# Optimization experiments

Hardware: AMD Instinct MI355X
Metric: run time of the kernel (lower is better)

## Reference

```python
import jax, jax.numpy as jnp
import numpy as np

N_HEADS = 16


def setup_inputs() -> dict:
    key = jax.random.key(0)
    ks = jax.random.split(key, 4)
    B, S, D = 2, 2048, 1024
    x = jax.random.normal(ks[0], (B, S, D), dtype=jnp.float32)
    scale = 1.0 / np.sqrt(D)
    Wq = jax.random.normal(ks[1], (D, D), dtype=jnp.float32) * scale
    Wk = jax.random.normal(ks[2], (D, D), dtype=jnp.float32) * scale
    Wv = jax.random.normal(ks[3], (D, D), dtype=jnp.float32) * scale
    bq = jnp.zeros((D,), jnp.float32)
    bk = jnp.zeros((D,), jnp.float32)
    bv = jnp.zeros((D,), jnp.float32)
    return {"x": x, "Wq": Wq, "bq": bq, "Wk": Wk, "bk": bk, "Wv": Wv, "bv": bv}


def _split_heads(t, n_heads):
    B, S, D = t.shape
    return t.reshape(B, S, n_heads, D // n_heads).transpose(0, 2, 1, 3)  # [B,H,S,hd]


def reference(x, Wq, bq, Wk, bk, Wv, bv):
    H = N_HEADS
    Q = _split_heads(x @ Wq + bq, H)
    K = _split_heads(x @ Wk + bk, H)
    V = _split_heads(x @ Wv + bv, H)
    head_size = Q.shape[-1]
    scores = jnp.einsum("bhqd,bhkd->bhqk", Q, K) / jnp.sqrt(jnp.float32(head_size))
    probs = jax.nn.softmax(scores, axis=-1)  # dropout p=0.01 -> identity in eval
    out = jnp.einsum("bhqk,bhkd->bhqd", probs, V)
    B, _, S, hd = out.shape
    return out.transpose(0, 2, 1, 3).reshape(B, S, H * hd)
```

## Files before the change

kernel.cpp:

```cpp
#include <hip/hip_runtime.h>
#include <hip/hip_bf16.h>

typedef __bf16 bf16x8 __attribute__((ext_vector_type(8)));
typedef __bf16 bf16x4 __attribute__((ext_vector_type(4)));
typedef float f32x4 __attribute__((ext_vector_type(4)));

#define B_ 2
#define S_ 2048
#define D_ 1024
#define H_ 16
#define HD_ 64
#define NT_ (S_ / 64)

__device__ inline void load_lds16(const __bf16* g, __bf16* l) {
  __builtin_amdgcn_global_load_lds(
      (const __attribute__((address_space(1))) void*)g,
      (__attribute__((address_space(3))) void*)l, 16, 0, 0);
}

__global__ __launch_bounds__(256) void prep(
    const float* __restrict__ X,
    const float* __restrict__ Wq, const float* __restrict__ Wk,
    const float* __restrict__ Wv,
    __bf16* __restrict__ Xb, __bf16* __restrict__ WT)
{
  const int z = blockIdx.z, t = threadIdx.x;
  if (z == 3) {
    size_t base = ((size_t)(blockIdx.y * 16 + blockIdx.x)) * 16384 + t * 4;
#pragma unroll
    for (int i = 0; i < 16; ++i) {
      size_t idx = base + (size_t)i * 1024;
      f32x4 v = *(const f32x4*)(X + idx);
      __bf16 o[4];
#pragma unroll
      for (int j = 0; j < 4; ++j) o[j] = (__bf16)v[j];
      *(ulong1*)(Xb + idx) = *(ulong1*)o;
    }
    return;
  }
  const float* W = (z == 0) ? Wq : (z == 1) ? Wk : Wv;
  __bf16* WTz = WT + (size_t)z * D_ * D_;
  const int k0 = blockIdx.y * 64, n0 = blockIdx.x * 64;

  __shared__ __bf16 T[64 * 72];
  {
    int kl = t >> 2, cg = (t & 3) * 16;
    const float* wp = W + (size_t)(k0 + kl) * D_ + n0 + cg;
    bf16x8 a, b;
#pragma unroll
    for (int j = 0; j < 4; ++j) { a[j] = (__bf16)wp[j];     a[4 + j] = (__bf16)wp[4 + j]; }
#pragma unroll
    for (int j = 0; j < 4; ++j) { b[j] = (__bf16)wp[8 + j]; b[4 + j] = (__bf16)wp[12 + j]; }
    *(bf16x8*)(T + kl * 72 + cg) = a;
    *(bf16x8*)(T + kl * 72 + cg + 8) = b;
  }
  __syncthreads();
  {
    int nl = t >> 2, kc = (t & 3) * 16;
    bf16x8 a, b;
#pragma unroll
    for (int j = 0; j < 8; ++j) a[j] = T[(kc + j) * 72 + nl];
#pragma unroll
    for (int j = 0; j < 8; ++j) b[j] = T[(kc + 8 + j) * 72 + nl];
    __bf16* op = WTz + (size_t)(n0 + nl) * D_ + k0 + kc;
    *(bf16x8*)(op) = a;
    *(bf16x8*)(op + 8) = b;
  }
}

__global__ __launch_bounds__(256) void qkv_gemm(
    const __bf16* __restrict__ Xb, const __bf16* __restrict__ WT,
    const float* __restrict__ bq, const float* __restrict__ bk,
    const float* __restrict__ bv,
    __bf16* __restrict__ Qw, __bf16* __restrict__ Kw, __bf16* __restrict__ VTw)
{
  const int z = blockIdx.z;
  const __bf16* Wz = WT + (size_t)z * D_ * D_;
  const float* bias = (z == 0) ? bq : (z == 1) ? bk : bv;
  __bf16* outp = (z == 0) ? Qw : (z == 1) ? Kw : VTw;
  const float mult = (z == 0) ? 0.125f * 1.44269504088896f : 1.0f;

  const int tid  = threadIdx.x;
  const int wave = tid >> 6, lane = tid & 63, ln = lane & 15, quad = lane >> 4;
  const int m0 = blockIdx.y * 128, n0 = blockIdx.x * 128;
  const int wm = (wave & 1) * 64, wn = (wave >> 1) * 64;

  __shared__ __bf16 Als[128 * 32];
  __shared__ __bf16 Bls[128 * 32];

  f32x4 acc[4][4] = {};

  for (int k0 = 0; k0 < D_; k0 += 32) {
    __syncthreads();
#pragma unroll
    for (int i = 0; i < 2; ++i) {
      int cb = wave * 128 + i * 64;
      int chunk = cb + lane;
      int row = chunk >> 2, c = chunk & 3;
      load_lds16(Xb + (size_t)(m0 + row) * D_ + k0 + c * 8, Als + cb * 8);
      load_lds16(Wz + (size_t)(n0 + row) * D_ + k0 + c * 8, Bls + cb * 8);
    }
    __syncthreads();

    bf16x8 af[4], bfr[4];
#pragma unroll
    for (int mt = 0; mt < 4; ++mt)
      af[mt] = *(const bf16x8*)(Als + (wm + mt * 16 + ln) * 32 + quad * 8);
#pragma unroll
    for (int nt = 0; nt < 4; ++nt)
      bfr[nt] = *(const bf16x8*)(Bls + (wn + nt * 16 + ln) * 32 + quad * 8);
#pragma unroll
    for (int mt = 0; mt < 4; ++mt)
#pragma unroll
      for (int nt = 0; nt < 4; ++nt)
        acc[mt][nt] = __builtin_amdgcn_mfma_f32_16x16x32_bf16(af[mt], bfr[nt], acc[mt][nt], 0, 0, 0);
  }

#pragma unroll
  for (int nt = 0; nt < 4; ++nt) {
    int n_g = n0 + wn + nt * 16 + ln;
    float bv_ = bias[n_g];
#pragma unroll
    for (int mt = 0; mt < 4; ++mt) {
#pragma unroll
      for (int r = 0; r < 4; ++r) {
        int m_g = m0 + wm + mt * 16 + quad * 4 + r;
        float c = (acc[mt][nt][r] + bv_) * mult;
        if (z < 2) {
          outp[(size_t)m_g * D_ + n_g] = (__bf16)c;
        } else {
          outp[(size_t)(m_g >> 11) * D_ * S_ + (size_t)n_g * S_ + (m_g & (S_ - 1))] = (__bf16)c;
        }
      }
    }
  }
}

__global__ __launch_bounds__(256) void attn(
    const __bf16* __restrict__ Q, const __bf16* __restrict__ K,
    const __bf16* __restrict__ VT, float* __restrict__ out)
{
  const int tid  = threadIdx.x;
  const int wave = tid >> 6, lane = tid & 63, ln = lane & 15, quad = lane >> 4;

  const int f = blockIdx.x;
  const int xcd = f & 7, g = f >> 3;
  const int bh = ((g & 3) << 3) | xcd;
  const int qt = g >> 2;
  const int b = bh >> 4, h = bh & 15;
  const int q0 = qt * 128 + wave * 32;

  const __bf16* Qbase = Q + (size_t)(b * S_ + q0) * D_ + h * HD_;
  bf16x8 qb[2][2];
#pragma unroll
  for (int nt = 0; nt < 2; ++nt)
#pragma unroll
    for (int ks = 0; ks < 2; ++ks)
      qb[nt][ks] = *(const bf16x8*)(Qbase + (size_t)(nt * 16 + ln) * D_ + ks * 32 + quad * 8);

  const __bf16* Kh = K + (size_t)b * S_ * D_ + h * HD_;
  const __bf16* Vh = VT + (size_t)(b * D_ + h * HD_) * S_;

  __shared__ __bf16 Kls[2][64 * 72];
  __shared__ __bf16 Vls[2][64 * 72];
  __shared__ __bf16 Pls[4][32 * 72];
  __shared__ float  Linv[4][32];
  __bf16* Pw = Pls[wave];

  f32x4 acc[2][4] = {};
  float lsum[2] = {0.f, 0.f};

  bf16x8 kreg[2], vreg[2];
#pragma unroll
  for (int i = 0; i < 2; ++i) {
    int chunk = i * 256 + tid, row = chunk >> 3, cc = chunk & 7;
    kreg[i] = *(const bf16x8*)(Kh + (size_t)row * D_ + cc * 8);
    vreg[i] = *(const bf16x8*)(Vh + (size_t)row * S_ + cc * 8);
  }

  for (int kt = 0; kt < NT_; ++kt) {
    __bf16* Kb = Kls[kt & 1];
    __bf16* Vb = Vls[kt & 1];
#pragma unroll
    for (int i = 0; i < 2; ++i) {
      int chunk = i * 256 + tid, row = chunk >> 3, cc = chunk & 7;
      *(bf16x8*)(Kb + row * 72 + cc * 8) = kreg[i];
      *(bf16x8*)(Vb + row * 72 + cc * 8) = vreg[i];
    }
    if (kt + 1 < NT_) {
#pragma unroll
      for (int i = 0; i < 2; ++i) {
        int chunk = i * 256 + tid, row = chunk >> 3, cc = chunk & 7;
        kreg[i] = *(const bf16x8*)(Kh + (size_t)((kt + 1) * 64 + row) * D_ + cc * 8);
        vreg[i] = *(const bf16x8*)(Vh + (size_t)row * S_ + (kt + 1) * 64 + cc * 8);
      }
    }
    __syncthreads();

    f32x4 st[4][2] = {};
#pragma unroll
    for (int mt = 0; mt < 4; ++mt) {
#pragma unroll
      for (int ks = 0; ks < 2; ++ks) {
        bf16x8 ka = *(const bf16x8*)(Kb + (mt * 16 + ln) * 72 + ks * 32 + quad * 8);
#pragma unroll
        for (int nt = 0; nt < 2; ++nt)
          st[mt][nt] = __builtin_amdgcn_mfma_f32_16x16x32_bf16(ka, qb[nt][ks], st[mt][nt], 0, 0, 0);
      }
    }

#pragma unroll
    for (int mt = 0; mt < 4; ++mt)
#pragma unroll
      for (int nt = 0; nt < 2; ++nt) {
        bf16x4 pk;
#pragma unroll
        for (int r = 0; r < 4; ++r) {
          float p = __builtin_amdgcn_exp2f(st[mt][nt][r]);
          lsum[nt] += p;
          pk[r] = (__bf16)p;
        }
        *(bf16x4*)(Pw + (nt * 16 + ln) * 72 + mt * 16 + quad * 4) = pk;
      }

#pragma unroll
    for (int ks = 0; ks < 2; ++ks) {
      bf16x8 pa[2];
#pragma unroll
      for (int mt = 0; mt < 2; ++mt)
        pa[mt] = *(const bf16x8*)(Pw + (mt * 16 + ln) * 72 + ks * 32 + quad * 8);
#pragma unroll
      for (int dt = 0; dt < 4; ++dt) {
        bf16x8 vb = *(const bf16x8*)(Vb + (dt * 16 + ln) * 72 + ks * 32 + quad * 8);
#pragma unroll
        for (int mt = 0; mt < 2; ++mt)
          acc[mt][dt] = __builtin_amdgcn_mfma_f32_16x16x32_bf16(pa[mt], vb, acc[mt][dt], 0, 0, 0);
      }
    }
    __syncthreads();
  }

#pragma unroll
  for (int nt = 0; nt < 2; ++nt) {
    lsum[nt] += __shfl_xor(lsum[nt], 16);
    lsum[nt] += __shfl_xor(lsum[nt], 32);
  }
  if (quad == 0) {
    Linv[wave][ln]      = 1.0f / lsum[0];
    Linv[wave][16 + ln] = 1.0f / lsum[1];
  }

#pragma unroll
  for (int mt = 0; mt < 2; ++mt)
#pragma unroll
    for (int r = 0; r < 4; ++r) {
      float li = Linv[wave][mt * 16 + quad * 4 + r];
      float* op = out + (size_t)(b * S_ + q0 + mt * 16 + quad * 4 + r) * D_ + h * HD_;
#pragma unroll
      for (int dt = 0; dt < 4; ++dt)
        op[dt * 16 + ln] = acc[mt][dt][r] * li;
    }
}

extern "C" void kernel_launch(void* const* d_in, const int* in_sizes, int n_in,
                              void* d_out, int out_size, void* d_ws, size_t ws_size,
                              hipStream_t stream) {
  const float* X  = (const float*)d_in[0];
  const float* Wq = (const float*)d_in[1];
  const float* bq = (const float*)d_in[2];
  const float* Wk = (const float*)d_in[3];
  const float* bk = (const float*)d_in[4];
  const float* Wv = (const float*)d_in[5];
  const float* bv = (const float*)d_in[6];

  __bf16* Qw  = (__bf16*)d_ws;
  __bf16* Kw  = Qw  + (size_t)B_ * S_ * D_;
  __bf16* VTw = Kw  + (size_t)B_ * S_ * D_;
  __bf16* Xb  = VTw + (size_t)B_ * S_ * D_;
  __bf16* WT  = Xb  + (size_t)B_ * S_ * D_;
  float* out = (float*)d_out;

  prep<<<dim3(16, 16, 4), 256, 0, stream>>>(X, Wq, Wk, Wv, Xb, WT);
  qkv_gemm<<<dim3(8, 32, 3), 256, 0, stream>>>(Xb, WT, bq, bk, bv, Qw, Kw, VTw);
  attn<<<512, 256, 0, stream>>>(Qw, Kw, VTw, out);
}
```

Before: 175.9 us.

## XOR-swizzle LDS tiles and compute softmax row sums via MFMA ones column

The GEMM and attention kernels drop padded LDS rows in favour of XOR-swizzled layouts, which saves LDS space while still avoiding bank conflicts on fragment reads. In attention, the V tile gains 16 constant rows of ones, so an extra MFMA column accumulates the softmax denominator. This replaces the per-element scalar lsum adds, the shuffles and the Linv LDS pass. The V-transpose output store in the projection kernel is vectorized to bf16x4. The trade-off is 25% more PV MFMA work in exchange for fewer VALU ops and less LDS footprint.

```diff
diff --git a/kernel.cpp b/kernel.cpp
--- a/kernel.cpp
+++ b/kernel.cpp
@@ -97,18 +97,20 @@
       int cb = wave * 128 + i * 64;
       int chunk = cb + lane;
       int row = chunk >> 2, c = chunk & 3;
-      load_lds16(Xb + (size_t)(m0 + row) * D_ + k0 + c * 8, Als + cb * 8);
-      load_lds16(Wz + (size_t)(n0 + row) * D_ + k0 + c * 8, Bls + cb * 8);
+      int gc = c ^ (row & 3);
+      load_lds16(Xb + (size_t)(m0 + row) * D_ + k0 + gc * 8, Als + cb * 8);
+      load_lds16(Wz + (size_t)(n0 + row) * D_ + k0 + gc * 8, Bls + cb * 8);
     }
     __syncthreads();
 
     bf16x8 af[4], bfr[4];
+    const int dsw = (quad ^ (ln & 3)) * 8;
 #pragma unroll
     for (int mt = 0; mt < 4; ++mt)
-      af[mt] = *(const bf16x8*)(Als + (wm + mt * 16 + ln) * 32 + quad * 8);
+      af[mt] = *(const bf16x8*)(Als + (wm + mt * 16 + ln) * 32 + dsw);
 #pragma unroll
     for (int nt = 0; nt < 4; ++nt)
-      bfr[nt] = *(const bf16x8*)(Bls + (wn + nt * 16 + ln) * 32 + quad * 8);
+      bfr[nt] = *(const bf16x8*)(Bls + (wn + nt * 16 + ln) * 32 + dsw);
 #pragma unroll
     for (int mt = 0; mt < 4; ++mt)
 #pragma unroll
@@ -122,15 +124,18 @@
     float bv_ = bias[n_g];
 #pragma unroll
     for (int mt = 0; mt < 4; ++mt) {
-#pragma unroll
-      for (int r = 0; r < 4; ++r) {
-        int m_g = m0 + wm + mt * 16 + quad * 4 + r;
-        float c = (acc[mt][nt][r] + bv_) * mult;
-        if (z < 2) {
-          outp[(size_t)m_g * D_ + n_g] = (__bf16)c;
-        } else {
-          outp[(size_t)(m_g >> 11) * D_ * S_ + (size_t)n_g * S_ + (m_g & (S_ - 1))] = (__bf16)c;
+      if (z < 2) {
+#pragma unroll
+        for (int r = 0; r < 4; ++r) {
+          int m_g = m0 + wm + mt * 16 + quad * 4 + r;
+          outp[(size_t)m_g * D_ + n_g] = (__bf16)((acc[mt][nt][r] + bv_) * mult);
         }
+      } else {
+        int m_g0 = m0 + wm + mt * 16 + quad * 4;
+        bf16x4 v4;
+#pragma unroll
+        for (int r = 0; r < 4; ++r) v4[r] = (__bf16)(acc[mt][nt][r] + bv_);
+        *(bf16x4*)(outp + (size_t)(m_g0 >> 11) * D_ * S_ + (size_t)n_g * S_ + (m_g0 & (S_ - 1))) = v4;
       }
     }
   }
@@ -161,14 +166,22 @@
   const __bf16* Kh = K + (size_t)b * S_ * D_ + h * HD_;
   const __bf16* Vh = VT + (size_t)(b * D_ + h * HD_) * S_;
 
-  __shared__ __bf16 Kls[2][64 * 72];
-  __shared__ __bf16 Vls[2][64 * 72];
-  __shared__ __bf16 Pls[4][32 * 72];
-  __shared__ float  Linv[4][32];
+  __shared__ __bf16 Kls[2][64 * 64];
+  __shared__ __bf16 Vls[2][80 * 64];
+  __shared__ __bf16 Pls[4][32 * 64];
   __bf16* Pw = Pls[wave];
 
-  f32x4 acc[2][4] = {};
-  float lsum[2] = {0.f, 0.f};
+  {
+    bf16x8 ones;
+#pragma unroll
+    for (int j = 0; j < 8; ++j) ones[j] = (__bf16)1.0f;
+    int buf = tid >> 7, rr = (tid >> 3) & 15, cc = tid & 7;
+    *(bf16x8*)(&Vls[buf][(64 + rr) * 64 + cc * 8]) = ones;
+  }
+
+  f32x4 acc[2][5] = {};
+
+  const int swl = ln & 7;
 
   bf16x8 kreg[2], vreg[2];
 #pragma unroll
@@ -184,8 +197,9 @@
 #pragma unroll
     for (int i = 0; i < 2; ++i) {
       int chunk = i * 256 + tid, row = chunk >> 3, cc = chunk & 7;
-      *(bf16x8*)(Kb + row * 72 + cc * 8) = kreg[i];
-      *(bf16x8*)(Vb + row * 72 + cc * 8) = vreg[i];
+      int sw = (cc ^ (row & 7)) * 8;
+      *(bf16x8*)(Kb + row * 64 + sw) = kreg[i];
+      *(bf16x8*)(Vb + row * 64 + sw) = vreg[i];
     }
     if (kt + 1 < NT_) {
 #pragma unroll
@@ -202,7 +216,7 @@
     for (int mt = 0; mt < 4; ++mt) {
 #pragma unroll
       for (int ks = 0; ks < 2; ++ks) {
-        bf16x8 ka = *(const bf16x8*)(Kb + (mt * 16 + ln) * 72 + ks * 32 + quad * 8);
+        bf16x8 ka = *(const bf16x8*)(Kb + (mt * 16 + ln) * 64 + ((ks * 4 + quad) ^ swl) * 8);
 #pragma unroll
         for (int nt = 0; nt < 2; ++nt)
           st[mt][nt] = __builtin_amdgcn_mfma_f32_16x16x32_bf16(ka, qb[nt][ks], st[mt][nt], 0, 0, 0);
@@ -215,12 +229,9 @@
       for (int nt = 0; nt < 2; ++nt) {
         bf16x4 pk;
 #pragma unroll
-        for (int r = 0; r < 4; ++r) {
-          float p = __builtin_amdgcn_exp2f(st[mt][nt][r]);
-          lsum[nt] += p;
-          pk[r] = (__bf16)p;
-        }
-        *(bf16x4*)(Pw + (nt * 16 + ln) * 72 + mt * 16 + quad * 4) = pk;
+        for (int r = 0; r < 4; ++r)
+          pk[r] = (__bf16)__builtin_amdgcn_exp2f(st[mt][nt][r]);
+        *(bf16x4*)(Pw + (nt * 16 + ln) * 64 + ((2 * mt + (quad >> 1)) ^ swl) * 8 + (quad & 1) * 4) = pk;
       }
 
 #pragma unroll
@@ -228,10 +239,11 @@
       bf16x8 pa[2];
 #pragma unroll
       for (int mt = 0; mt < 2; ++mt)
-        pa[mt] = *(const bf16x8*)(Pw + (mt * 16 + ln) * 72 + ks * 32 + quad * 8);
-#pragma unroll
-      for (int dt = 0; dt < 4; ++dt) {
-        bf16x8 vb = *(const bf16x8*)(Vb + (dt * 16 + ln) * 72 + ks * 32 + quad * 8);
+        pa[mt] = *(const bf16x8*)(Pw + (mt * 16 + ln) * 64 + ((ks * 4 + quad) ^ swl) * 8);
+#pragma unroll
+      for (int dt = 0; dt < 5; ++dt) {
+        int vrow = (dt < 4) ? dt * 16 + ln : 64 + ln;
+        bf16x8 vb = *(const bf16x8*)(Vb + vrow * 64 + ((ks * 4 + quad) ^ swl) * 8);
 #pragma unroll
         for (int mt = 0; mt < 2; ++mt)
           acc[mt][dt] = __builtin_amdgcn_mfma_f32_16x16x32_bf16(pa[mt], vb, acc[mt][dt], 0, 0, 0);
@@ -241,20 +253,10 @@
   }
 
 #pragma unroll
-  for (int nt = 0; nt < 2; ++nt) {
-    lsum[nt] += __shfl_xor(lsum[nt], 16);
-    lsum[nt] += __shfl_xor(lsum[nt], 32);
-  }
-  if (quad == 0) {
-    Linv[wave][ln]      = 1.0f / lsum[0];
-    Linv[wave][16 + ln] = 1.0f / lsum[1];
-  }
-
-#pragma unroll
   for (int mt = 0; mt < 2; ++mt)
 #pragma unroll
     for (int r = 0; r < 4; ++r) {
-      float li = Linv[wave][mt * 16 + quad * 4 + r];
+      float li = 1.0f / acc[mt][4][r];
       float* op = out + (size_t)(b * S_ + q0 + mt * 16 + quad * 4 + r) * D_ + h * HD_;
 #pragma unroll
       for (int dt = 0; dt < 4; ++dt)
```

Measured after the change: 168.9 us. -4.0%, faster.
